# Kernel optimization log

Hardware: AMD Instinct MI355X
Metric: run time of the kernel (lower is better)

The kernel has to match this reference:

```python
import jax, jax.numpy as jnp
import numpy as np

N, IN_C, OUT_C = 4096, 256, 64
ALPHA = 0.2  # LeakyReLU negative slope


def setup_inputs() -> dict:
    key = jax.random.key(0)
    k1, k2, k3, k4 = jax.random.split(key, 4)
    H = jax.random.normal(k1, (N, IN_C), dtype=jnp.float32)
    adj = jax.random.randint(k2, (N, N), 0, 2, dtype=jnp.int32)
    # xavier_uniform with gain=1.414
    gain = 1.414
    limW = gain * np.sqrt(6.0 / (IN_C + OUT_C))
    W = jax.random.uniform(k3, (IN_C, OUT_C), minval=-limW, maxval=limW, dtype=jnp.float32)
    lima = gain * np.sqrt(6.0 / (2 * OUT_C + 1))
    a = jax.random.uniform(k4, (2 * OUT_C, 1), minval=-lima, maxval=lima, dtype=jnp.float32)
    return {"H": H, "adj": adj, "W": W, "a": a}


def reference(H, adj, W, a):
    Wh = H @ W  # [N, out_C]
    # Attention_Mat[i,j] = concat(Wh_i, Wh_j); score = Attention_Mat @ a
    # = (Wh @ a1)_i + (Wh @ a2)_j  -- fused, avoids the O(N^2 * 2F) tensor.
    a1, a2 = a[:OUT_C, 0], a[OUT_C:, 0]
    e = (Wh @ a1)[:, None] + (Wh @ a2)[None, :]  # [N, N]
    e = jnp.where(e > 0, e, ALPHA * e)  # LeakyReLU
    att = jax.nn.softmax(e, axis=1)
    # NOTE: original masks AFTER softmax (rows are not renormalized).
    att = jnp.where(adj > 0, att, jnp.zeros_like(att))
    out = att @ Wh  # [N, out_C]
    return jax.nn.elu(out)  # concat=True
```

## Files before the change

### kernel.cpp

```cpp
#include <hip/hip_runtime.h>
#include <math.h>

static constexpr int NN   = 4096;
static constexpr int INC  = 256;
static constexpr int OUTC = 64;
#define LRELU_ALPHA 0.2f

__device__ __forceinline__ float lrelu(float x) {
    return fmaxf(x, 0.f) + LRELU_ALPHA * fminf(x, 0.f);
}
__device__ __forceinline__ float elu1(float x) {
    return x > 0.f ? x : (__expf(x) - 1.f);
}

__global__ __launch_bounds__(256) void k_wh(const float* __restrict__ H,
                                            const float* __restrict__ W,
                                            const float* __restrict__ a,
                                            float* __restrict__ Wh,
                                            float* __restrict__ f1,
                                            float* __restrict__ f2) {
    __shared__ __align__(16) float Wl[INC * OUTC];
    __shared__ __align__(16) float Hl[16 * INC];
    const int t = threadIdx.x;
    const int i0 = blockIdx.x * 16;
    {
        const float4* W4 = (const float4*)W;
        float4* Wl4 = (float4*)Wl;
        #pragma unroll
        for (int u = 0; u < 16; ++u) Wl4[u * 256 + t] = W4[u * 256 + t];
        const float4* H4 = (const float4*)(H + i0 * INC);
        float4* Hl4 = (float4*)Hl;
        #pragma unroll
        for (int u = 0; u < 4; ++u) Hl4[u * 256 + t] = H4[u * 256 + t];
    }
    __syncthreads();
    const int c = t & 63;
    const int g = t >> 6;
    const float a1c = a[c];
    const float a2c = a[OUTC + c];
    float acc[4] = {0.f, 0.f, 0.f, 0.f};
    const float4* Hl4 = (const float4*)Hl;
    for (int k4 = 0; k4 < INC / 4; ++k4) {
        const float w0 = Wl[(k4 * 4 + 0) * OUTC + c];
        const float w1 = Wl[(k4 * 4 + 1) * OUTC + c];
        const float w2 = Wl[(k4 * 4 + 2) * OUTC + c];
        const float w3 = Wl[(k4 * 4 + 3) * OUTC + c];
        #pragma unroll
        for (int s = 0; s < 4; ++s) {
            const float4 h = Hl4[(g + 4 * s) * (INC / 4) + k4];
            acc[s] = fmaf(h.x, w0, fmaf(h.y, w1, fmaf(h.z, w2, fmaf(h.w, w3, acc[s]))));
        }
    }
    #pragma unroll
    for (int s = 0; s < 4; ++s) {
        const int r = g + 4 * s;
        Wh[(i0 + r) * OUTC + c] = acc[s];
        float v1 = acc[s] * a1c;
        float v2 = acc[s] * a2c;
        #pragma unroll
        for (int off = 32; off; off >>= 1) {
            v1 += __shfl_xor(v1, off);
            v2 += __shfl_xor(v2, off);
        }
        if (c == 0) { f1[i0 + r] = v1; f2[i0 + r] = v2; }
    }
}

__global__ __launch_bounds__(256) void k_max(const float* __restrict__ f2,
                                             float* __restrict__ mx) {
    __shared__ float red[4];
    const int t = threadIdx.x;
    float m = -3.4e38f;
    for (int idx = t; idx < NN; idx += 256) m = fmaxf(m, f2[idx]);
    #pragma unroll
    for (int off = 32; off; off >>= 1) m = fmaxf(m, __shfl_xor(m, off));
    if ((t & 63) == 0) red[t >> 6] = m;
    __syncthreads();
    if (t == 0) mx[0] = fmaxf(fmaxf(red[0], red[1]), fmaxf(red[2], red[3]));
}

__global__ __launch_bounds__(256) void k_att(const int* __restrict__ adj,
                                             const float* __restrict__ Wh,
                                             const float* __restrict__ f1,
                                             const float* __restrict__ f2,
                                             const float* __restrict__ mx,
                                             float* __restrict__ numP,
                                             float* __restrict__ denP) {
    __shared__ __align__(16) float pm[64 * 68];
    __shared__ __align__(16) float wh[64 * 64];
    const int t = threadIdx.x;
    const int rt = blockIdx.x >> 3;
    const int js = blockIdx.x & 7;
    const int i0 = rt * 64;
    const int j0b = js * 512;
    const int q    = t & 15;
    const int rowg = t >> 4;
    const float maxf2 = mx[0];
    float f1r[4], mrow[4];
    #pragma unroll
    for (int s = 0; s < 4; ++s) {
        const float v = f1[i0 + rowg + 16 * s];
        f1r[s] = v;
        mrow[s] = lrelu(v + maxf2);
    }
    float dacc[4] = {0.f, 0.f, 0.f, 0.f};
    float4 acc[4];
    #pragma unroll
    for (int s = 0; s < 4; ++s) acc[s] = make_float4(0.f, 0.f, 0.f, 0.f);

    const float4* Wh4 = (const float4*)Wh;
    float4* wh4 = (float4*)wh;
    const float4* pm4 = (const float4*)pm;
    const int4* adj4 = (const int4*)adj;
    const float4* f24 = (const float4*)f2;

    for (int tile = 0; tile < 8; ++tile) {
        const int j0 = j0b + tile * 64;
        #pragma unroll
        for (int u = 0; u < 4; ++u) {
            const int idx = u * 256 + t;
            wh4[idx] = Wh4[j0 * 16 + idx];
        }
        const float4 f2v = f24[(j0 >> 2) + q];
        #pragma unroll
        for (int s = 0; s < 4; ++s) {
            const int r = rowg + 16 * s;
            const int4 av = adj4[(((i0 + r) * NN + j0) >> 2) + q];
            const float p0 = __expf(lrelu(f1r[s] + f2v.x) - mrow[s]);
            const float p1 = __expf(lrelu(f1r[s] + f2v.y) - mrow[s]);
            const float p2 = __expf(lrelu(f1r[s] + f2v.z) - mrow[s]);
            const float p3 = __expf(lrelu(f1r[s] + f2v.w) - mrow[s]);
            dacc[s] += (p0 + p1 + p2 + p3);
            float4 st;
            st.x = av.x > 0 ? p0 : 0.f;
            st.y = av.y > 0 ? p1 : 0.f;
            st.z = av.z > 0 ? p2 : 0.f;
            st.w = av.w > 0 ? p3 : 0.f;
            *(float4*)&pm[r * 68 + 4 * q] = st;
        }
        __syncthreads();
        for (int qq = 0; qq < 16; ++qq) {
            const float4 w0 = wh4[(qq * 4 + 0) * 16 + q];
            const float4 w1 = wh4[(qq * 4 + 1) * 16 + q];
            const float4 w2 = wh4[(qq * 4 + 2) * 16 + q];
            const float4 w3 = wh4[(qq * 4 + 3) * 16 + q];
            #pragma unroll
            for (int s = 0; s < 4; ++s) {
                const float4 p4 = pm4[(rowg + 16 * s) * 17 + qq];
                acc[s].x = fmaf(p4.x, w0.x, fmaf(p4.y, w1.x, fmaf(p4.z, w2.x, fmaf(p4.w, w3.x, acc[s].x))));
                acc[s].y = fmaf(p4.x, w0.y, fmaf(p4.y, w1.y, fmaf(p4.z, w2.y, fmaf(p4.w, w3.y, acc[s].y))));
                acc[s].z = fmaf(p4.x, w0.z, fmaf(p4.y, w1.z, fmaf(p4.z, w2.z, fmaf(p4.w, w3.z, acc[s].z))));
                acc[s].w = fmaf(p4.x, w0.w, fmaf(p4.y, w1.w, fmaf(p4.z, w2.w, fmaf(p4.w, w3.w, acc[s].w))));
            }
        }
        __syncthreads();
    }
    float4* numP4 = (float4*)numP;
    #pragma unroll
    for (int s = 0; s < 4; ++s) {
        const int r = rowg + 16 * s;
        numP4[(js * NN + i0 + r) * 16 + q] = acc[s];
        float v = dacc[s];
        v += __shfl_xor(v, 1);
        v += __shfl_xor(v, 2);
        v += __shfl_xor(v, 4);
        v += __shfl_xor(v, 8);
        if (q == 0) denP[js * NN + i0 + r] = v;
    }
}

__global__ __launch_bounds__(256) void k_fin(const float* __restrict__ numP,
                                             const float* __restrict__ denP,
                                             float* __restrict__ out) {
    const int id = blockIdx.x * 256 + threadIdx.x;
    const int i = id >> 4;
    const int c4 = id & 15;
    const float4* n4 = (const float4*)numP;
    float4 s = make_float4(0.f, 0.f, 0.f, 0.f);
    float den = 0.f;
    #pragma unroll
    for (int p = 0; p < 8; ++p) {
        const float4 v = n4[(p * NN + i) * 16 + c4];
        s.x += v.x; s.y += v.y; s.z += v.z; s.w += v.w;
        den += denP[p * NN + i];
    }
    const float inv = 1.f / den;
    float4 o;
    o.x = elu1(s.x * inv);
    o.y = elu1(s.y * inv);
    o.z = elu1(s.z * inv);
    o.w = elu1(s.w * inv);
    ((float4*)out)[id] = o;
}

extern "C" void kernel_launch(void* const* d_in, const int* in_sizes, int n_in,
                              void* d_out, int out_size, void* d_ws, size_t ws_size,
                              hipStream_t stream) {
    const float* H  = (const float*)d_in[0];
    const int* adj  = (const int*)d_in[1];
    const float* W  = (const float*)d_in[2];
    const float* a  = (const float*)d_in[3];
    float* out = (float*)d_out;
    char* ws = (char*)d_ws;
    float* Wh   = (float*)(ws);
    float* f1   = (float*)(ws + (1 << 20));
    float* f2   = (float*)(ws + (1 << 20) + (16 << 10));
    float* mx   = (float*)(ws + (1 << 20) + (32 << 10));
    float* denP = (float*)(ws + (1 << 20) + (64 << 10));
    float* numP = (float*)(ws + (1 << 20) + (256 << 10));
    hipLaunchKernelGGL(k_wh,  dim3(256), dim3(256), 0, stream, H, W, a, Wh, f1, f2);
    hipLaunchKernelGGL(k_max, dim3(1),   dim3(256), 0, stream, f2, mx);
    hipLaunchKernelGGL(k_att, dim3(512), dim3(256), 0, stream, adj, Wh, f1, f2, mx, numP, denP);
    hipLaunchKernelGGL(k_fin, dim3(256), dim3(256), 0, stream, numP, denP, out);
}
```

Before: 139.2 us.

## Use fp16 MFMA for attention aggregation with transposed half-precision Wh

The attention-times-Wh product moves from scalar FP32 FMAs through shared memory to MFMA 16x16x32 f16 instructions. k_wh now writes Wh transposed and in half precision so each lane can load an 8-wide B fragment directly. k_att is reorganised so each block covers 16 rows and half of the columns across 8 waves, with partial results reduced in shared memory, and k_fin sums 2 partials instead of 8. The goal is to remove the FP32 compute bottleneck and the per-tile LDS staging, at the cost of fp16 rounding of both the probabilities and Wh.

```diff
diff --git a/kernel.cpp b/kernel.cpp
--- a/kernel.cpp
+++ b/kernel.cpp
@@ -4,10 +4,12 @@
 static constexpr int NN   = 4096;
 static constexpr int INC  = 256;
 static constexpr int OUTC = 64;
-#define LRELU_ALPHA 0.2f
+
+typedef _Float16 half8 __attribute__((ext_vector_type(8)));
+typedef float floatx4 __attribute__((ext_vector_type(4)));
 
 __device__ __forceinline__ float lrelu(float x) {
-    return fmaxf(x, 0.f) + LRELU_ALPHA * fminf(x, 0.f);
+    return fmaxf(x, 0.f) + 0.2f * fminf(x, 0.f);
 }
 __device__ __forceinline__ float elu1(float x) {
     return x > 0.f ? x : (__expf(x) - 1.f);
@@ -16,11 +18,12 @@
 __global__ __launch_bounds__(256) void k_wh(const float* __restrict__ H,
                                             const float* __restrict__ W,
                                             const float* __restrict__ a,
-                                            float* __restrict__ Wh,
+                                            unsigned short* __restrict__ WhT,
                                             float* __restrict__ f1,
                                             float* __restrict__ f2) {
     __shared__ __align__(16) float Wl[INC * OUTC];
     __shared__ __align__(16) float Hl[16 * INC];
+    __shared__ _Float16 Tl[16 * 68];
     const int t = threadIdx.x;
     const int i0 = blockIdx.x * 16;
     {
@@ -54,7 +57,7 @@
     #pragma unroll
     for (int s = 0; s < 4; ++s) {
         const int r = g + 4 * s;
-        Wh[(i0 + r) * OUTC + c] = acc[s];
+        Tl[r * 68 + c] = (_Float16)acc[s];
         float v1 = acc[s] * a1c;
         float v2 = acc[s] * a2c;
         #pragma unroll
@@ -64,6 +67,15 @@
         }
         if (c == 0) { f1[i0 + r] = v1; f2[i0 + r] = v2; }
     }
+    __syncthreads();
+    const int c2 = t >> 2;
+    const int rs = (t & 3) * 4;
+    ushort4 u;
+    u.x = *(const unsigned short*)&Tl[(rs + 0) * 68 + c2];
+    u.y = *(const unsigned short*)&Tl[(rs + 1) * 68 + c2];
+    u.z = *(const unsigned short*)&Tl[(rs + 2) * 68 + c2];
+    u.w = *(const unsigned short*)&Tl[(rs + 3) * 68 + c2];
+    *(ushort4*)(WhT + c2 * NN + i0 + rs) = u;
 }
 
 __global__ __launch_bounds__(256) void k_max(const float* __restrict__ f2,
@@ -71,7 +83,11 @@
     __shared__ float red[4];
     const int t = threadIdx.x;
     float m = -3.4e38f;
-    for (int idx = t; idx < NN; idx += 256) m = fmaxf(m, f2[idx]);
+    const float4* f24 = (const float4*)f2;
+    for (int idx = t; idx < NN / 4; idx += 256) {
+        const float4 v = f24[idx];
+        m = fmaxf(m, fmaxf(fmaxf(v.x, v.y), fmaxf(v.z, v.w)));
+    }
     #pragma unroll
     for (int off = 32; off; off >>= 1) m = fmaxf(m, __shfl_xor(m, off));
     if ((t & 63) == 0) red[t >> 6] = m;
@@ -79,93 +95,75 @@
     if (t == 0) mx[0] = fmaxf(fmaxf(red[0], red[1]), fmaxf(red[2], red[3]));
 }
 
-__global__ __launch_bounds__(256) void k_att(const int* __restrict__ adj,
-                                             const float* __restrict__ Wh,
-                                             const float* __restrict__ f1,
-                                             const float* __restrict__ f2,
-                                             const float* __restrict__ mx,
-                                             float* __restrict__ numP,
-                                             float* __restrict__ denP) {
-    __shared__ __align__(16) float pm[64 * 68];
-    __shared__ __align__(16) float wh[64 * 64];
+__global__ __launch_bounds__(512, 4) void k_att(const int* __restrict__ adj,
+                                                const _Float16* __restrict__ WhT,
+                                                const float* __restrict__ f1,
+                                                const float* __restrict__ f2,
+                                                const float* __restrict__ mx,
+                                                float* __restrict__ numP,
+                                                float* __restrict__ denP) {
+    __shared__ float sacc[8 * 1024];
+    __shared__ float sden[8 * 16];
     const int t = threadIdx.x;
-    const int rt = blockIdx.x >> 3;
-    const int js = blockIdx.x & 7;
-    const int i0 = rt * 64;
-    const int j0b = js * 512;
-    const int q    = t & 15;
-    const int rowg = t >> 4;
+    const int w = t >> 6;
+    const int l = t & 63;
+    const int m = l & 15;
+    const int quad = l >> 4;
+    const int rb = blockIdx.x >> 1;
+    const int js = blockIdx.x & 1;
+    const int i0 = rb * 16;
     const float maxf2 = mx[0];
-    float f1r[4], mrow[4];
+    const float f1r = f1[i0 + m];
+    const float mrow = lrelu(f1r + maxf2);
+    float den = 0.f;
+    floatx4 acc[4] = {{0.f,0.f,0.f,0.f},{0.f,0.f,0.f,0.f},{0.f,0.f,0.f,0.f},{0.f,0.f,0.f,0.f}};
+    const int jbase = js * 2048 + w * 32 + quad * 8;
+    const int* adjrow = adj + (size_t)(i0 + m) * NN;
+
+    for (int it = 0; it < 8; ++it) {
+        const int j = jbase + it * 256;
+        const int4 a0 = *(const int4*)(adjrow + j);
+        const int4 a1 = *(const int4*)(adjrow + j + 4);
+        const float4 g0 = *(const float4*)(f2 + j);
+        const float4 g1 = *(const float4*)(f2 + j + 4);
+        half8 af;
+        {
+            float p;
+            p = __expf(lrelu(f1r + g0.x) - mrow); den += p; af[0] = (a0.x > 0) ? (_Float16)p : (_Float16)0.f;
+            p = __expf(lrelu(f1r + g0.y) - mrow); den += p; af[1] = (a0.y > 0) ? (_Float16)p : (_Float16)0.f;
+            p = __expf(lrelu(f1r + g0.z) - mrow); den += p; af[2] = (a0.z > 0) ? (_Float16)p : (_Float16)0.f;
+            p = __expf(lrelu(f1r + g0.w) - mrow); den += p; af[3] = (a0.w > 0) ? (_Float16)p : (_Float16)0.f;
+            p = __expf(lrelu(f1r + g1.x) - mrow); den += p; af[4] = (a1.x > 0) ? (_Float16)p : (_Float16)0.f;
+            p = __expf(lrelu(f1r + g1.y) - mrow); den += p; af[5] = (a1.y > 0) ? (_Float16)p : (_Float16)0.f;
+            p = __expf(lrelu(f1r + g1.z) - mrow); den += p; af[6] = (a1.z > 0) ? (_Float16)p : (_Float16)0.f;
+            p = __expf(lrelu(f1r + g1.w) - mrow); den += p; af[7] = (a1.w > 0) ? (_Float16)p : (_Float16)0.f;
+        }
+        #pragma unroll
+        for (int nt = 0; nt < 4; ++nt) {
+            const half8 bf = *(const half8*)(WhT + (size_t)(nt * 16 + m) * NN + j);
+            acc[nt] = __builtin_amdgcn_mfma_f32_16x16x32_f16(af, bf, acc[nt], 0, 0, 0);
+        }
+    }
+    den += __shfl_xor(den, 16);
+    den += __shfl_xor(den, 32);
+    if (l < 16) sden[w * 16 + l] = den;
     #pragma unroll
-    for (int s = 0; s < 4; ++s) {
-        const float v = f1[i0 + rowg + 16 * s];
-        f1r[s] = v;
-        mrow[s] = lrelu(v + maxf2);
-    }
-    float dacc[4] = {0.f, 0.f, 0.f, 0.f};
-    float4 acc[4];
-    #pragma unroll
-    for (int s = 0; s < 4; ++s) acc[s] = make_float4(0.f, 0.f, 0.f, 0.f);
-
-    const float4* Wh4 = (const float4*)Wh;
-    float4* wh4 = (float4*)wh;
-    const float4* pm4 = (const float4*)pm;
-    const int4* adj4 = (const int4*)adj;
-    const float4* f24 = (const float4*)f2;
-
-    for (int tile = 0; tile < 8; ++tile) {
-        const int j0 = j0b + tile * 64;
-        #pragma unroll
-        for (int u = 0; u < 4; ++u) {
-            const int idx = u * 256 + t;
-            wh4[idx] = Wh4[j0 * 16 + idx];
-        }
-        const float4 f2v = f24[(j0 >> 2) + q];
-        #pragma unroll
-        for (int s = 0; s < 4; ++s) {
-            const int r = rowg + 16 * s;
-            const int4 av = adj4[(((i0 + r) * NN + j0) >> 2) + q];
-            const float p0 = __expf(lrelu(f1r[s] + f2v.x) - mrow[s]);
-            const float p1 = __expf(lrelu(f1r[s] + f2v.y) - mrow[s]);
-            const float p2 = __expf(lrelu(f1r[s] + f2v.z) - mrow[s]);
-            const float p3 = __expf(lrelu(f1r[s] + f2v.w) - mrow[s]);
-            dacc[s] += (p0 + p1 + p2 + p3);
-            float4 st;
-            st.x = av.x > 0 ? p0 : 0.f;
-            st.y = av.y > 0 ? p1 : 0.f;
-            st.z = av.z > 0 ? p2 : 0.f;
-            st.w = av.w > 0 ? p3 : 0.f;
-            *(float4*)&pm[r * 68 + 4 * q] = st;
-        }
-        __syncthreads();
-        for (int qq = 0; qq < 16; ++qq) {
-            const float4 w0 = wh4[(qq * 4 + 0) * 16 + q];
-            const float4 w1 = wh4[(qq * 4 + 1) * 16 + q];
-            const float4 w2 = wh4[(qq * 4 + 2) * 16 + q];
-            const float4 w3 = wh4[(qq * 4 + 3) * 16 + q];
-            #pragma unroll
-            for (int s = 0; s < 4; ++s) {
-                const float4 p4 = pm4[(rowg + 16 * s) * 17 + qq];
-                acc[s].x = fmaf(p4.x, w0.x, fmaf(p4.y, w1.x, fmaf(p4.z, w2.x, fmaf(p4.w, w3.x, acc[s].x))));
-                acc[s].y = fmaf(p4.x, w0.y, fmaf(p4.y, w1.y, fmaf(p4.z, w2.y, fmaf(p4.w, w3.y, acc[s].y))));
-                acc[s].z = fmaf(p4.x, w0.z, fmaf(p4.y, w1.z, fmaf(p4.z, w2.z, fmaf(p4.w, w3.z, acc[s].z))));
-                acc[s].w = fmaf(p4.x, w0.w, fmaf(p4.y, w1.w, fmaf(p4.z, w2.w, fmaf(p4.w, w3.w, acc[s].w))));
-            }
-        }
-        __syncthreads();
-    }
-    float4* numP4 = (float4*)numP;
-    #pragma unroll
-    for (int s = 0; s < 4; ++s) {
-        const int r = rowg + 16 * s;
-        numP4[(js * NN + i0 + r) * 16 + q] = acc[s];
-        float v = dacc[s];
-        v += __shfl_xor(v, 1);
-        v += __shfl_xor(v, 2);
-        v += __shfl_xor(v, 4);
-        v += __shfl_xor(v, 8);
-        if (q == 0) denP[js * NN + i0 + r] = v;
+    for (int nt = 0; nt < 4; ++nt)
+        #pragma unroll
+        for (int r = 0; r < 4; ++r)
+            sacc[w * 1024 + (quad * 4 + r) * 64 + nt * 16 + m] = acc[nt][r];
+    __syncthreads();
+    for (int o = t; o < 1024; o += 512) {
+        float s = 0.f;
+        #pragma unroll
+        for (int w2 = 0; w2 < 8; ++w2) s += sacc[w2 * 1024 + o];
+        numP[(size_t)js * NN * 64 + i0 * 64 + o] = s;
+    }
+    if (t < 16) {
+        float s = 0.f;
+        #pragma unroll
+        for (int w2 = 0; w2 < 8; ++w2) s += sden[w2 * 16 + t];
+        denP[js * NN + i0 + t] = s;
     }
 }
 
@@ -174,22 +172,16 @@
                                              float* __restrict__ out) {
     const int id = blockIdx.x * 256 + threadIdx.x;
     const int i = id >> 4;
-    const int c4 = id & 15;
     const float4* n4 = (const float4*)numP;
-    float4 s = make_float4(0.f, 0.f, 0.f, 0.f);
-    float den = 0.f;
-    #pragma unroll
-    for (int p = 0; p < 8; ++p) {
-        const float4 v = n4[(p * NN + i) * 16 + c4];
-        s.x += v.x; s.y += v.y; s.z += v.z; s.w += v.w;
-        den += denP[p * NN + i];
-    }
+    const float4 v0 = n4[id];
+    const float4 v1 = n4[id + NN * 16];
+    const float den = denP[i] + denP[NN + i];
     const float inv = 1.f / den;
     float4 o;
-    o.x = elu1(s.x * inv);
-    o.y = elu1(s.y * inv);
-    o.z = elu1(s.z * inv);
-    o.w = elu1(s.w * inv);
+    o.x = elu1((v0.x + v1.x) * inv);
+    o.y = elu1((v0.y + v1.y) * inv);
+    o.z = elu1((v0.z + v1.z) * inv);
+    o.w = elu1((v0.w + v1.w) * inv);
     ((float4*)out)[id] = o;
 }
 
@@ -202,14 +194,14 @@
     const float* a  = (const float*)d_in[3];
     float* out = (float*)d_out;
     char* ws = (char*)d_ws;
-    float* Wh   = (float*)(ws);
-    float* f1   = (float*)(ws + (1 << 20));
-    float* f2   = (float*)(ws + (1 << 20) + (16 << 10));
-    float* mx   = (float*)(ws + (1 << 20) + (32 << 10));
-    float* denP = (float*)(ws + (1 << 20) + (64 << 10));
-    float* numP = (float*)(ws + (1 << 20) + (256 << 10));
-    hipLaunchKernelGGL(k_wh,  dim3(256), dim3(256), 0, stream, H, W, a, Wh, f1, f2);
+    unsigned short* WhT = (unsigned short*)(ws);
+    float* f1   = (float*)(ws + (512 << 10));
+    float* f2   = (float*)(ws + (528 << 10));
+    float* mx   = (float*)(ws + (544 << 10));
+    float* denP = (float*)(ws + (560 << 10));
+    float* numP = (float*)(ws + (1 << 20));
+    hipLaunchKernelGGL(k_wh,  dim3(256), dim3(256), 0, stream, H, W, a, WhT, f1, f2);
     hipLaunchKernelGGL(k_max, dim3(1),   dim3(256), 0, stream, f2, mx);
-    hipLaunchKernelGGL(k_att, dim3(512), dim3(256), 0, stream, adj, Wh, f1, f2, mx, numP, denP);
+    hipLaunchKernelGGL(k_att, dim3(512), dim3(512), 0, stream, adj, (const _Float16*)WhT, f1, f2, mx, numP, denP);
     hipLaunchKernelGGL(k_fin, dim3(256), dim3(256), 0, stream, numP, denP, out);
 }
```

Result: faster. 129.9 us (-6.7%).
